# Kernel tuning notes

Hardware: AMD Instinct MI355X
Metric: run time of the kernel (lower is better)

Reference implementation:

```python
import jax, jax.numpy as jnp
import numpy as np

N_NODES = 100000


def _gcn_conv(x, W, b, src, dst, num_nodes):
    """PyG-style GCNConv: add self-loops, symmetric normalization, linear.
    x: [N, Fin], W: [Fin, Fout], b: [Fout], src/dst: [E] (already include self-loops).
    """
    h = x @ W  # [N, Fout] transform first (PyG order), keeps edge traffic at Fout width
    ones = jnp.ones(dst.shape[0], dtype=h.dtype)
    deg = jax.ops.segment_sum(ones, dst, num_segments=num_nodes)  # degree of A+I
    dinv = jnp.where(deg > 0, jax.lax.rsqrt(deg), 0.0)
    norm = dinv[src] * dinv[dst]  # [E]
    msg = h[src] * norm[:, None]  # [E, Fout] gather + scale
    out = jax.ops.segment_sum(msg, dst, num_segments=num_nodes)  # scatter-add
    return out + b


def setup_inputs() -> dict:
    key = jax.random.key(0)
    k1, k2, k3, k4, k5 = jax.random.split(key, 5)
    input_dim, hidden_dim, embedding_dim = 128, 64, 32
    x = jax.random.normal(k1, (N_NODES, input_dim), dtype=jnp.float32)
    edge_index = jax.random.randint(k2, (2, 1600000), 0, N_NODES, dtype=jnp.int32)
    # Glorot-like init for weights
    W1 = jax.random.normal(k3, (input_dim, hidden_dim), dtype=jnp.float32) / np.sqrt(input_dim)
    b1 = jnp.zeros((hidden_dim,), dtype=jnp.float32)
    W2 = jax.random.normal(k4, (hidden_dim, embedding_dim), dtype=jnp.float32) / np.sqrt(hidden_dim)
    b2 = jnp.zeros((embedding_dim,), dtype=jnp.float32)
    return {"x": x, "edge_index": edge_index, "W1": W1, "b1": b1, "W2": W2, "b2": b2}


def reference(x, edge_index, W1, b1, W2, b2):
    num_nodes = x.shape[0]
    loop = jnp.arange(num_nodes, dtype=edge_index.dtype)
    src = jnp.concatenate([edge_index[0], loop])  # add self-loops (PyG default)
    dst = jnp.concatenate([edge_index[1], loop])
    h = _gcn_conv(x, W1, b1, src, dst, num_nodes)
    h = jax.nn.relu(h)
    z = _gcn_conv(h, W2, b2, src, dst, num_nodes)
    return z
```

## Files before the change

### kernel.cpp

```cpp
#include <hip/hip_runtime.h>
#include <hip/hip_bf16.h>


#define MAXBUCK 512
#define CURSTRIDE 16

typedef unsigned int uint32;

__device__ __forceinline__ void fma4(float4& a, float s, const float4& w) {
    a.x = fmaf(s, w.x, a.x); a.y = fmaf(s, w.y, a.y);
    a.z = fmaf(s, w.z, a.z); a.w = fmaf(s, w.w, a.w);
}
__device__ __forceinline__ uint32 bf16rn(float f) {
    uint32 u = __float_as_uint(f);
    return (u + 0x7fffu + ((u >> 16) & 1u)) >> 16;
}
__device__ __forceinline__ float bflo(uint32 v) { return __uint_as_float(v << 16); }
__device__ __forceinline__ float bfhi(uint32 v) { return __uint_as_float(v & 0xffff0000u); }

__global__ void k_initcur(int* __restrict__ cursor, int nbuck, int cap) {
    int i = blockIdx.x * blockDim.x + threadIdx.x;
    if (i < nbuck) cursor[i * CURSTRIDE] = i * cap;
}

__global__ __launch_bounds__(1024) void k_bin(const int* __restrict__ src,
                                              const int* __restrict__ dst, int E,
                                              int nbuck, int cap,
                                              int* __restrict__ cursor,
                                              uint32* __restrict__ pairs) {
    __shared__ int hist[MAXBUCK];
    __shared__ int base_l[MAXBUCK];
    __shared__ int cur[MAXBUCK];
    int t = threadIdx.x;
    int e0 = blockIdx.x * 4096;
    for (int i = t; i < MAXBUCK; i += 1024) { hist[i] = 0; cur[i] = 0; }
    __syncthreads();
    for (int i = t; i < 4096; i += 1024) {
        int e = e0 + i;
        if (e < E) atomicAdd(&hist[dst[e] >> 8], 1);
    }
    __syncthreads();
    for (int i = t; i < nbuck; i += 1024)
        base_l[i] = hist[i] ? atomicAdd(&cursor[i * CURSTRIDE], hist[i]) : 0;
    __syncthreads();
    for (int i = t; i < 4096; i += 1024) {
        int e = e0 + i;
        if (e < E) {
            int d = dst[e];
            int b = d >> 8;
            int p = atomicAdd(&cur[b], 1);
            int idx = base_l[b] + p;
            if (idx < (b + 1) * cap)
                pairs[idx] = (uint32)src[e] | ((uint32)(d & 255) << 24);
        }
    }
}

__global__ __launch_bounds__(1024) void k_fill2(const uint32* __restrict__ pairs,
                                                const int* __restrict__ bucket_end,
                                                int cap, int N,
                                                int* __restrict__ srclist,
                                                int* __restrict__ rowstart,
                                                int* __restrict__ cnt,
                                                float* __restrict__ dinv) {
    __shared__ int hist[256];
    __shared__ int sh[256];
    __shared__ int rs_ex[256];
    __shared__ int cur[256];
    int b = blockIdx.x;
    int t = threadIdx.x;
    int start = b * cap;
    int end = min(bucket_end[b * CURSTRIDE], start + cap);
    int node0 = b << 8;

    if (t < 256) { hist[t] = 0; cur[t] = 0; }
    __syncthreads();
    for (int e = start + t; e < end; e += 1024)
        atomicAdd(&hist[pairs[e] >> 24], 1);
    __syncthreads();
    int v = 0;
    if (t < 256) { v = hist[t]; sh[t] = v; }
    __syncthreads();
    for (int off = 1; off < 256; off <<= 1) {
        int tmp = 0;
        if (t < 256 && t >= off) tmp = sh[t - off];
        __syncthreads();
        if (t < 256) sh[t] += tmp;
        __syncthreads();
    }
    if (t < 256) {
        rs_ex[t] = sh[t] - v;
        int node = node0 + t;
        if (node < N) {
            rowstart[node] = start + rs_ex[t];
            cnt[node] = v;
            dinv[node] = rsqrtf((float)(v + 1));
        }
    }
    __syncthreads();
    for (int e = start + t; e < end; e += 1024) {
        uint32 pr = pairs[e];
        int dl = pr >> 24;
        int p = atomicAdd(&cur[dl], 1);
        srclist[start + rs_ex[dl] + p] = (int)(pr & 0x00FFFFFFu);
    }
}

__global__ __launch_bounds__(256) void k_gemm1(const float* __restrict__ x,
                                               const float* __restrict__ W1,
                                               const float* __restrict__ dinv,
                                               uint32* __restrict__ h1b, int n) {
    __shared__ float W1s[128 * 64];
    __shared__ float xs[32][132];
    int t = threadIdx.x;
    const float4* W1v = (const float4*)W1;
    float4* W1sv = (float4*)W1s;
    for (int i = t; i < 2048; i += 256) W1sv[i] = W1v[i];
    int node0 = blockIdx.x * 32;
    const float4* xv = (const float4*)x;
    for (int i = t; i < 1024; i += 256) {
        int nl = i >> 5, kq = i & 31;
        int node = node0 + nl;
        float4 v = make_float4(0.f, 0.f, 0.f, 0.f);
        if (node < n) v = xv[(size_t)node * 32 + kq];
        *(float4*)&xs[nl][kq * 4] = v;
    }
    __syncthreads();

    int tx = t & 15;
    int ty = t >> 4;
    int na = ty * 2, nb = na + 1;
    float4 acc0 = make_float4(0.f, 0.f, 0.f, 0.f);
    float4 acc1 = make_float4(0.f, 0.f, 0.f, 0.f);
    const float4* W1sq = (const float4*)W1s;
#pragma unroll 4
    for (int kq = 0; kq < 32; kq++) {
        float4 xa = *(const float4*)&xs[na][kq * 4];
        float4 xb = *(const float4*)&xs[nb][kq * 4];
        float4 w0 = W1sq[(kq * 4 + 0) * 16 + tx];
        float4 w1 = W1sq[(kq * 4 + 1) * 16 + tx];
        float4 w2 = W1sq[(kq * 4 + 2) * 16 + tx];
        float4 w3 = W1sq[(kq * 4 + 3) * 16 + tx];
        fma4(acc0, xa.x, w0); fma4(acc0, xa.y, w1);
        fma4(acc0, xa.z, w2); fma4(acc0, xa.w, w3);
        fma4(acc1, xb.x, w0); fma4(acc1, xb.y, w1);
        fma4(acc1, xb.z, w2); fma4(acc1, xb.w, w3);
    }
    int nA = node0 + na, nB = node0 + nb;
    if (nA < n) {
        float di = dinv[nA];
        uint2 pk = make_uint2(bf16rn(acc0.x * di) | (bf16rn(acc0.y * di) << 16),
                              bf16rn(acc0.z * di) | (bf16rn(acc0.w * di) << 16));
        ((uint2*)h1b)[(size_t)nA * 16 + tx] = pk;
    }
    if (nB < n) {
        float di = dinv[nB];
        uint2 pk = make_uint2(bf16rn(acc1.x * di) | (bf16rn(acc1.y * di) << 16),
                              bf16rn(acc1.z * di) | (bf16rn(acc1.w * di) << 16));
        ((uint2*)h1b)[(size_t)nB * 16 + tx] = pk;
    }
}

__global__ __launch_bounds__(256) void k_gather_l1(const int* __restrict__ rowstart,
                                                   const int* __restrict__ cnt,
                                                   const int* __restrict__ srclist,
                                                   const uint32* __restrict__ h1b,
                                                   const float* __restrict__ dinv,
                                                   const float* __restrict__ b1,
                                                   const float* __restrict__ W2,
                                                   unsigned short* __restrict__ h2b, int n) {
    __shared__ __align__(16) float W2s[64 * 32];
    __shared__ __align__(16) float hb[8][64];
    int t = threadIdx.x;
    {
        const float4* W2v = (const float4*)W2;
        float4* W2sv = (float4*)W2s;
        W2sv[t] = W2v[t];
        W2sv[t + 256] = W2v[t + 256];
    }
    int wid = t >> 6, lane = t & 63;
    int nodeA = blockIdx.x * 8 + wid * 2;
    int nodeB = nodeA + 1;
    bool validA = (nodeA < n), validB = (nodeB < n);
    int j = lane & 15, q = lane >> 4;

    int rowA = 0, mA = 0, rowB = 0, mB = 0;
    float diA = 0.0f, diB = 0.0f;
    uint2 svA = make_uint2(0u, 0u), svB = make_uint2(0u, 0u);
    const uint2* h1v = (const uint2*)h1b;
    if (validA) { rowA = rowstart[nodeA]; mA = cnt[nodeA]; diA = dinv[nodeA];
                  svA = h1v[(size_t)nodeA * 16 + j]; }
    if (validB) { rowB = rowstart[nodeB]; mB = cnt[nodeB]; diB = dinv[nodeB];
                  svB = h1v[(size_t)nodeB * 16 + j]; }
    int mA0 = min(64, mA), mB0 = min(64, mB);
    int sidxA = (lane < mA0) ? srclist[rowA + lane] : 0;
    int sidxB = (lane < mB0) ? srclist[rowB + lane] : 0;

    float aA0 = 0.f, aA1 = 0.f, aA2 = 0.f, aA3 = 0.f;
    float aB0 = 0.f, aB1 = 0.f, aB2 = 0.f, aB3 = 0.f;
    int jjA = 0, jjB = 0;
    for (; jjA + 16 <= mA0 && jjB + 16 <= mB0; jjA += 16, jjB += 16) {
        int sA0 = __shfl(sidxA, jjA + q),      sA1 = __shfl(sidxA, jjA + 4 + q);
        int sA2 = __shfl(sidxA, jjA + 8 + q),  sA3 = __shfl(sidxA, jjA + 12 + q);
        int sB0 = __shfl(sidxB, jjB + q),      sB1 = __shfl(sidxB, jjB + 4 + q);
        int sB2 = __shfl(sidxB, jjB + 8 + q),  sB3 = __shfl(sidxB, jjB + 12 + q);
        uint2 vA0 = h1v[(size_t)sA0 * 16 + j], vA1 = h1v[(size_t)sA1 * 16 + j];
        uint2 vA2 = h1v[(size_t)sA2 * 16 + j], vA3 = h1v[(size_t)sA3 * 16 + j];
        uint2 vB0 = h1v[(size_t)sB0 * 16 + j], vB1 = h1v[(size_t)sB1 * 16 + j];
        uint2 vB2 = h1v[(size_t)sB2 * 16 + j], vB3 = h1v[(size_t)sB3 * 16 + j];
        aA0 += (bflo(vA0.x) + bflo(vA1.x)) + (bflo(vA2.x) + bflo(vA3.x));
        aA1 += (bfhi(vA0.x) + bfhi(vA1.x)) + (bfhi(vA2.x) + bfhi(vA3.x));
        aA2 += (bflo(vA0.y) + bflo(vA1.y)) + (bflo(vA2.y) + bflo(vA3.y));
        aA3 += (bfhi(vA0.y) + bfhi(vA1.y)) + (bfhi(vA2.y) + bfhi(vA3.y));
        aB0 += (bflo(vB0.x) + bflo(vB1.x)) + (bflo(vB2.x) + bflo(vB3.x));
        aB1 += (bfhi(vB0.x) + bfhi(vB1.x)) + (bfhi(vB2.x) + bfhi(vB3.x));
        aB2 += (bflo(vB0.y) + bflo(vB1.y)) + (bflo(vB2.y) + bflo(vB3.y));
        aB3 += (bfhi(vB0.y) + bfhi(vB1.y)) + (bfhi(vB2.y) + bfhi(vB3.y));
    }
    for (; jjA + 8 <= mA0 && jjB + 8 <= mB0; jjA += 8, jjB += 8) {
        int sA0 = __shfl(sidxA, jjA + q), sA1 = __shfl(sidxA, jjA + 4 + q);
        int sB0 = __shfl(sidxB, jjB + q), sB1 = __shfl(sidxB, jjB + 4 + q);
        uint2 vA0 = h1v[(size_t)sA0 * 16 + j], vA1 = h1v[(size_t)sA1 * 16 + j];
        uint2 vB0 = h1v[(size_t)sB0 * 16 + j], vB1 = h1v[(size_t)sB1 * 16 + j];
        aA0 += bflo(vA0.x) + bflo(vA1.x);
        aA1 += bfhi(vA0.x) + bfhi(vA1.x);
        aA2 += bflo(vA0.y) + bflo(vA1.y);
        aA3 += bfhi(vA0.y) + bfhi(vA1.y);
        aB0 += bflo(vB0.x) + bflo(vB1.x);
        aB1 += bfhi(vB0.x) + bfhi(vB1.x);
        aB2 += bflo(vB0.y) + bflo(vB1.y);
        aB3 += bfhi(vB0.y) + bfhi(vB1.y);
    }
    for (; jjA + 8 <= mA0; jjA += 8) {
        int s0 = __shfl(sidxA, jjA + q), s1 = __shfl(sidxA, jjA + 4 + q);
        uint2 v0 = h1v[(size_t)s0 * 16 + j], v1 = h1v[(size_t)s1 * 16 + j];
        aA0 += bflo(v0.x) + bflo(v1.x);
        aA1 += bfhi(v0.x) + bfhi(v1.x);
        aA2 += bflo(v0.y) + bflo(v1.y);
        aA3 += bfhi(v0.y) + bfhi(v1.y);
    }
    for (; jjA < mA0; jjA += 4) {
        int jidx = jjA + q;
        int s = __shfl(sidxA, min(jidx, mA0 - 1));
        uint2 v = h1v[(size_t)s * 16 + j];
        if (jidx < mA0) {
            aA0 += bflo(v.x); aA1 += bfhi(v.x);
            aA2 += bflo(v.y); aA3 += bfhi(v.y);
        }
    }
    for (; jjB + 8 <= mB0; jjB += 8) {
        int s0 = __shfl(sidxB, jjB + q), s1 = __shfl(sidxB, jjB + 4 + q);
        uint2 v0 = h1v[(size_t)s0 * 16 + j], v1 = h1v[(size_t)s1 * 16 + j];
        aB0 += bflo(v0.x) + bflo(v1.x);
        aB1 += bfhi(v0.x) + bfhi(v1.x);
        aB2 += bflo(v0.y) + bflo(v1.y);
        aB3 += bfhi(v0.y) + bfhi(v1.y);
    }
    for (; jjB < mB0; jjB += 4) {
        int jidx = jjB + q;
        int s = __shfl(sidxB, min(jidx, mB0 - 1));
        uint2 v = h1v[(size_t)s * 16 + j];
        if (jidx < mB0) {
            aB0 += bflo(v.x); aB1 += bfhi(v.x);
            aB2 += bflo(v.y); aB3 += bfhi(v.y);
        }
    }
    for (int j0 = 64; j0 < mA; j0 += 64) {
        int m = min(64, mA - j0);
        int sb = (lane < m) ? srclist[rowA + j0 + lane] : 0;
        int jj = 0;
        for (; jj + 8 <= m; jj += 8) {
            int s0 = __shfl(sb, jj + q), s1 = __shfl(sb, jj + 4 + q);
            uint2 v0 = h1v[(size_t)s0 * 16 + j], v1 = h1v[(size_t)s1 * 16 + j];
            aA0 += bflo(v0.x) + bflo(v1.x);
            aA1 += bfhi(v0.x) + bfhi(v1.x);
            aA2 += bflo(v0.y) + bflo(v1.y);
            aA3 += bfhi(v0.y) + bfhi(v1.y);
        }
        for (; jj < m; jj += 4) {
            int jidx = jj + q;
            int s = __shfl(sb, min(jidx, m - 1));
            uint2 v = h1v[(size_t)s * 16 + j];
            if (jidx < m) {
                aA0 += bflo(v.x); aA1 += bfhi(v.x);
                aA2 += bflo(v.y); aA3 += bfhi(v.y);
            }
        }
    }
    for (int j0 = 64; j0 < mB; j0 += 64) {
        int m = min(64, mB - j0);
        int sb = (lane < m) ? srclist[rowB + j0 + lane] : 0;
        int jj = 0;
        for (; jj + 8 <= m; jj += 8) {
            int s0 = __shfl(sb, jj + q), s1 = __shfl(sb, jj + 4 + q);
            uint2 v0 = h1v[(size_t)s0 * 16 + j], v1 = h1v[(size_t)s1 * 16 + j];
            aB0 += bflo(v0.x) + bflo(v1.x);
            aB1 += bfhi(v0.x) + bfhi(v1.x);
            aB2 += bflo(v0.y) + bflo(v1.y);
            aB3 += bfhi(v0.y) + bfhi(v1.y);
        }
        for (; jj < m; jj += 4) {
            int jidx = jj + q;
            int s = __shfl(sb, min(jidx, m - 1));
            uint2 v = h1v[(size_t)s * 16 + j];
            if (jidx < m) {
                aB0 += bflo(v.x); aB1 += bfhi(v.x);
                aB2 += bflo(v.y); aB3 += bfhi(v.y);
            }
        }
    }

    aA0 += __shfl_xor(aA0, 16); aA0 += __shfl_xor(aA0, 32);
    aA1 += __shfl_xor(aA1, 16); aA1 += __shfl_xor(aA1, 32);
    aA2 += __shfl_xor(aA2, 16); aA2 += __shfl_xor(aA2, 32);
    aA3 += __shfl_xor(aA3, 16); aA3 += __shfl_xor(aA3, 32);
    aB0 += __shfl_xor(aB0, 16); aB0 += __shfl_xor(aB0, 32);
    aB1 += __shfl_xor(aB1, 16); aB1 += __shfl_xor(aB1, 32);
    aB2 += __shfl_xor(aB2, 16); aB2 += __shfl_xor(aB2, 32);
    aB3 += __shfl_xor(aB3, 16); aB3 += __shfl_xor(aB3, 32);
    if (validA && q == 0) {
        float4 bq = ((const float4*)b1)[j];
        float4 hv;
        hv.x = fmaxf((aA0 + bflo(svA.x)) * diA + bq.x, 0.0f);
        hv.y = fmaxf((aA1 + bfhi(svA.x)) * diA + bq.y, 0.0f);
        hv.z = fmaxf((aA2 + bflo(svA.y)) * diA + bq.z, 0.0f);
        hv.w = fmaxf((aA3 + bfhi(svA.y)) * diA + bq.w, 0.0f);
        *(float4*)&hb[wid * 2][4 * j] = hv;
    }
    if (validB && q == 0) {
        float4 bq = ((const float4*)b1)[j];
        float4 hv;
        hv.x = fmaxf((aB0 + bflo(svB.x)) * diB + bq.x, 0.0f);
        hv.y = fmaxf((aB1 + bfhi(svB.x)) * diB + bq.y, 0.0f);
        hv.z = fmaxf((aB2 + bflo(svB.y)) * diB + bq.z, 0.0f);
        hv.w = fmaxf((aB3 + bfhi(svB.y)) * diB + bq.w, 0.0f);
        *(float4*)&hb[wid * 2 + 1][4 * j] = hv;
    }
    __syncthreads();
    int c = lane & 31, half = lane >> 5;
    int k0 = half * 32;
    if (validA) {
        float s = 0.0f;
        const float4* hb4 = (const float4*)&hb[wid * 2][k0];
#pragma unroll
        for (int kk = 0; kk < 8; kk++) {
            float4 h4 = hb4[kk];
            int kb = k0 + kk * 4;
            s = fmaf(h4.x, W2s[(kb + 0) * 32 + c], s);
            s = fmaf(h4.y, W2s[(kb + 1) * 32 + c], s);
            s = fmaf(h4.z, W2s[(kb + 2) * 32 + c], s);
            s = fmaf(h4.w, W2s[(kb + 3) * 32 + c], s);
        }
        s += __shfl_xor(s, 32);
        if (half == 0) h2b[(size_t)nodeA * 32 + c] = (unsigned short)bf16rn(s * diA);
    }
    if (validB) {
        float s = 0.0f;
        const float4* hb4 = (const float4*)&hb[wid * 2 + 1][k0];
#pragma unroll
        for (int kk = 0; kk < 8; kk++) {
            float4 h4 = hb4[kk];
            int kb = k0 + kk * 4;
            s = fmaf(h4.x, W2s[(kb + 0) * 32 + c], s);
            s = fmaf(h4.y, W2s[(kb + 1) * 32 + c], s);
            s = fmaf(h4.z, W2s[(kb + 2) * 32 + c], s);
            s = fmaf(h4.w, W2s[(kb + 3) * 32 + c], s);
        }
        s += __shfl_xor(s, 32);
        if (half == 0) h2b[(size_t)nodeB * 32 + c] = (unsigned short)bf16rn(s * diB);
    }
}

__global__ __launch_bounds__(256) void k_gather_l2(const int* __restrict__ rowstart,
                                                   const int* __restrict__ cnt,
                                                   const int* __restrict__ srclist,
                                                   const uint32* __restrict__ h2b,
                                                   const float* __restrict__ dinv,
                                                   const float* __restrict__ b2v,
                                                   float* __restrict__ out, int n) {
    int t = threadIdx.x;
    int wid = t >> 6, lane = t & 63;
    int nodeA = blockIdx.x * 8 + wid * 2;
    if (nodeA >= n) return;
    int nodeB = nodeA + 1;
    bool validB = (nodeB < n);
    int j = lane & 7, o = lane >> 3;

    int rowA = rowstart[nodeA], mA = cnt[nodeA];
    float diA = dinv[nodeA];
    int rowB = 0, mB = 0;
    float diB = 0.0f;
    const uint2* h2v = (const uint2*)h2b;
    uint2 svA = h2v[(size_t)nodeA * 8 + j];
    uint2 svB = make_uint2(0u, 0u);
    if (validB) { rowB = rowstart[nodeB]; mB = cnt[nodeB]; diB = dinv[nodeB];
                  svB = h2v[(size_t)nodeB * 8 + j]; }
    int mA0 = min(64, mA), mB0 = min(64, mB);
    int sidxA = (lane < mA0) ? srclist[rowA + lane] : 0;
    int sidxB = (lane < mB0) ? srclist[rowB + lane] : 0;

    float aA0 = 0.f, aA1 = 0.f, aA2 = 0.f, aA3 = 0.f;
    float aB0 = 0.f, aB1 = 0.f, aB2 = 0.f, aB3 = 0.f;
    int jjA = 0, jjB = 0;
    for (; jjA + 16 <= mA0 && jjB + 16 <= mB0; jjA += 16, jjB += 16) {
        int sA0 = __shfl(sidxA, jjA + o), sA1 = __shfl(sidxA, jjA + 8 + o);
        int sB0 = __shfl(sidxB, jjB + o), sB1 = __shfl(sidxB, jjB + 8 + o);
        uint2 vA0 = h2v[(size_t)sA0 * 8 + j], vA1 = h2v[(size_t)sA1 * 8 + j];
        uint2 vB0 = h2v[(size_t)sB0 * 8 + j], vB1 = h2v[(size_t)sB1 * 8 + j];
        aA0 += bflo(vA0.x) + bflo(vA1.x);
        aA1 += bfhi(vA0.x) + bfhi(vA1.x);
        aA2 += bflo(vA0.y) + bflo(vA1.y);
        aA3 += bfhi(vA0.y) + bfhi(vA1.y);
        aB0 += bflo(vB0.x) + bflo(vB1.x);
        aB1 += bfhi(vB0.x) + bfhi(vB1.x);
        aB2 += bflo(vB0.y) + bflo(vB1.y);
        aB3 += bfhi(vB0.y) + bfhi(vB1.y);
    }
    for (; jjA + 8 <= mA0 && jjB + 8 <= mB0; jjA += 8, jjB += 8) {
        int sA0 = __shfl(sidxA, jjA + o);
        int sB0 = __shfl(sidxB, jjB + o);
        uint2 vA0 = h2v[(size_t)sA0 * 8 + j];
        uint2 vB0 = h2v[(size_t)sB0 * 8 + j];
        aA0 += bflo(vA0.x); aA1 += bfhi(vA0.x);
        aA2 += bflo(vA0.y); aA3 += bfhi(vA0.y);
        aB0 += bflo(vB0.x); aB1 += bfhi(vB0.x);
        aB2 += bflo(vB0.y); aB3 += bfhi(vB0.y);
    }
    for (; jjA + 8 <= mA0; jjA += 8) {
        int s0 = __shfl(sidxA, jjA + o);
        uint2 v0 = h2v[(size_t)s0 * 8 + j];
        aA0 += bflo(v0.x); aA1 += bfhi(v0.x);
        aA2 += bflo(v0.y); aA3 += bfhi(v0.y);
    }
    if (jjA < mA0) {
        int jidx = jjA + o;
        int s = __shfl(sidxA, min(jidx, mA0 - 1));
        uint2 v = h2v[(size_t)s * 8 + j];
        if (jidx < mA0) {
            aA0 += bflo(v.x); aA1 += bfhi(v.x);
            aA2 += bflo(v.y); aA3 += bfhi(v.y);
        }
    }
    for (; jjB + 8 <= mB0; jjB += 8) {
        int s0 = __shfl(sidxB, jjB + o);
        uint2 v0 = h2v[(size_t)s0 * 8 + j];
        aB0 += bflo(v0.x); aB1 += bfhi(v0.x);
        aB2 += bflo(v0.y); aB3 += bfhi(v0.y);
    }
    if (jjB < mB0) {
        int jidx = jjB + o;
        int s = __shfl(sidxB, min(jidx, mB0 - 1));
        uint2 v = h2v[(size_t)s * 8 + j];
        if (jidx < mB0) {
            aB0 += bflo(v.x); aB1 += bfhi(v.x);
            aB2 += bflo(v.y); aB3 += bfhi(v.y);
        }
    }
    for (int j0 = 64; j0 < mA; j0 += 64) {
        int m = min(64, mA - j0);
        int sb = (lane < m) ? srclist[rowA + j0 + lane] : 0;
        int jj = 0;
        for (; jj + 8 <= m; jj += 8) {
            int s0 = __shfl(sb, jj + o);
            uint2 v0 = h2v[(size_t)s0 * 8 + j];
            aA0 += bflo(v0.x); aA1 += bfhi(v0.x);
            aA2 += bflo(v0.y); aA3 += bfhi(v0.y);
        }
        if (jj < m) {
            int jidx = jj + o;
            int s = __shfl(sb, min(jidx, m - 1));
            uint2 v = h2v[(size_t)s * 8 + j];
            if (jidx < m) {
                aA0 += bflo(v.x); aA1 += bfhi(v.x);
                aA2 += bflo(v.y); aA3 += bfhi(v.y);
            }
        }
    }
    for (int j0 = 64; j0 < mB; j0 += 64) {
        int m = min(64, mB - j0);
        int sb = (lane < m) ? srclist[rowB + j0 + lane] : 0;
        int jj = 0;
        for (; jj + 8 <= m; jj += 8) {
            int s0 = __shfl(sb, jj + o);
            uint2 v0 = h2v[(size_t)s0 * 8 + j];
            aB0 += bflo(v0.x); aB1 += bfhi(v0.x);
            aB2 += bflo(v0.y); aB3 += bfhi(v0.y);
        }
        if (jj < m) {
            int jidx = jj + o;
            int s = __shfl(sb, min(jidx, m - 1));
            uint2 v = h2v[(size_t)s * 8 + j];
            if (jidx < m) {
                aB0 += bflo(v.x); aB1 += bfhi(v.x);
                aB2 += bflo(v.y); aB3 += bfhi(v.y);
            }
        }
    }

    a_reduce:
    aA0 += __shfl_xor(aA0, 8); aA0 += __shfl_xor(aA0, 16); aA0 += __shfl_xor(aA0, 32);
    aA1 += __shfl_xor(aA1, 8); aA1 += __shfl_xor(aA1, 16); aA1 += __shfl_xor(aA1, 32);
    aA2 += __shfl_xor(aA2, 8); aA2 += __shfl_xor(aA2, 16); aA2 += __shfl_xor(aA2, 32);
    aA3 += __shfl_xor(aA3, 8); aA3 += __shfl_xor(aA3, 16); aA3 += __shfl_xor(aA3, 32);
    aB0 += __shfl_xor(aB0, 8); aB0 += __shfl_xor(aB0, 16); aB0 += __shfl_xor(aB0, 32);
    aB1 += __shfl_xor(aB1, 8); aB1 += __shfl_xor(aB1, 16); aB1 += __shfl_xor(aB1, 32);
    aB2 += __shfl_xor(aB2, 8); aB2 += __shfl_xor(aB2, 16); aB2 += __shfl_xor(aB2, 32);
    aB3 += __shfl_xor(aB3, 8); aB3 += __shfl_xor(aB3, 16); aB3 += __shfl_xor(aB3, 32);
    if (o == 0) {
        float4 bq = ((const float4*)b2v)[j];
        float4 ov;
        ov.x = (aA0 + bflo(svA.x)) * diA + bq.x;
        ov.y = (aA1 + bfhi(svA.x)) * diA + bq.y;
        ov.z = (aA2 + bflo(svA.y)) * diA + bq.z;
        ov.w = (aA3 + bfhi(svA.y)) * diA + bq.w;
        ((float4*)out)[(size_t)nodeA * 8 + j] = ov;
        if (validB) {
            float4 ob;
            ob.x = (aB0 + bflo(svB.x)) * diB + bq.x;
            ob.y = (aB1 + bfhi(svB.x)) * diB + bq.y;
            ob.z = (aB2 + bflo(svB.y)) * diB + bq.z;
            ob.w = (aB3 + bfhi(svB.y)) * diB + bq.w;
            ((float4*)out)[(size_t)nodeB * 8 + j] = ob;
        }
    }
}

extern "C" void kernel_launch(void* const* d_in, const int* in_sizes, int n_in,
                              void* d_out, int out_size, void* d_ws, size_t ws_size,
                              hipStream_t stream) {
    const float* x  = (const float*)d_in[0];
    const int*   ei = (const int*)d_in[1];
    const float* W1 = (const float*)d_in[2];
    const float* b1 = (const float*)d_in[3];
    const float* W2 = (const float*)d_in[4];
    const float* b2 = (const float*)d_in[5];
    float* out = (float*)d_out;

    const int N = in_sizes[0] / 128;
    const int E = in_sizes[1] / 2;
    const int* src = ei;
    const int* dst = ei + E;
    const int nbuck = (N + 255) >> 8;

    int mean = (E + nbuck - 1) / nbuck;
    int cap = (mean + (mean >> 3) + 256 + 63) & ~63;
    size_t region = (size_t)nbuck * cap;

    char* p = (char*)d_ws;
    uint32* pairs      = (uint32*)p;    p += region * 4;
    int* srclist       = (int*)p;       p += region * 4;
    uint32* h1b        = (uint32*)p;    p += (size_t)N * 64 * 2;
    uint32* h2b        = (uint32*)p;    p += (size_t)N * 32 * 2;
    int* cursor        = (int*)p;       p += MAXBUCK * CURSTRIDE * 4;
    int* rowstart      = (int*)p;       p += (size_t)N * 4;
    int* cnt           = (int*)p;       p += (size_t)N * 4;
    float* dinv        = (float*)p;     p += (size_t)N * 4;

    k_initcur<<<(nbuck + 255) / 256, 256, 0, stream>>>(cursor, nbuck, cap);
    k_bin<<<(E + 4095) / 4096, 1024, 0, stream>>>(src, dst, E, nbuck, cap, cursor, pairs);
    k_fill2<<<nbuck, 1024, 0, stream>>>(pairs, cursor, cap, N, srclist, rowstart, cnt, dinv);

    k_gemm1<<<(N + 31) / 32, 256, 0, stream>>>(x, W1, dinv, h1b, N);
    k_gather_l1<<<(N + 7) / 8, 256, 0, stream>>>(rowstart, cnt, srclist, h1b, dinv,
                                                 b1, W2, (unsigned short*)h2b, N);
    k_gather_l2<<<(N + 7) / 8, 256, 0, stream>>>(rowstart, cnt, srclist, h2b, dinv,
                                                 b2, out, N);
}
```

Baseline: 235.7 us.

## Halve gemm1 shared memory, cache dst in LDS, replace cursor init kernel with memset

k_gemm1 now stages W1 and x in two K-halves, cutting shared memory per block from about 49KB to about 25KB so more blocks can be resident, at the cost of an extra sync phase. k_bin keeps the dst values in shared memory so it does not re-read them from global memory. The cursor-init kernel is replaced by a memset, with bucket offsets added inside k_bin, and k_fill2 now reads per-bucket counts instead of end positions.

Measured after the change: 234.3 us. No clear change (-0.6%).

```diff
diff --git a/kernel.cpp b/kernel.cpp
--- a/kernel.cpp
+++ b/kernel.cpp
@@ -17,11 +17,6 @@
 }
 __device__ __forceinline__ float bflo(uint32 v) { return __uint_as_float(v << 16); }
 __device__ __forceinline__ float bfhi(uint32 v) { return __uint_as_float(v & 0xffff0000u); }
-
-__global__ void k_initcur(int* __restrict__ cursor, int nbuck, int cap) {
-    int i = blockIdx.x * blockDim.x + threadIdx.x;
-    if (i < nbuck) cursor[i * CURSTRIDE] = i * cap;
-}
 
 __global__ __launch_bounds__(1024) void k_bin(const int* __restrict__ src,
                                               const int* __restrict__ dst, int E,
@@ -31,22 +26,27 @@
     __shared__ int hist[MAXBUCK];
     __shared__ int base_l[MAXBUCK];
     __shared__ int cur[MAXBUCK];
+    __shared__ int dloc[4096];
     int t = threadIdx.x;
     int e0 = blockIdx.x * 4096;
     for (int i = t; i < MAXBUCK; i += 1024) { hist[i] = 0; cur[i] = 0; }
-    __syncthreads();
-    for (int i = t; i < 4096; i += 1024) {
-        int e = e0 + i;
-        if (e < E) atomicAdd(&hist[dst[e] >> 8], 1);
-    }
-    __syncthreads();
-    for (int i = t; i < nbuck; i += 1024)
-        base_l[i] = hist[i] ? atomicAdd(&cursor[i * CURSTRIDE], hist[i]) : 0;
     __syncthreads();
     for (int i = t; i < 4096; i += 1024) {
         int e = e0 + i;
         if (e < E) {
             int d = dst[e];
+            dloc[i] = d;
+            atomicAdd(&hist[d >> 8], 1);
+        }
+    }
+    __syncthreads();
+    for (int i = t; i < nbuck; i += 1024)
+        base_l[i] = hist[i] ? (i * cap + atomicAdd(&cursor[i * CURSTRIDE], hist[i])) : 0;
+    __syncthreads();
+    for (int i = t; i < 4096; i += 1024) {
+        int e = e0 + i;
+        if (e < E) {
+            int d = dloc[i];
             int b = d >> 8;
             int p = atomicAdd(&cur[b], 1);
             int idx = base_l[b] + p;
@@ -57,7 +57,7 @@
 }
 
 __global__ __launch_bounds__(1024) void k_fill2(const uint32* __restrict__ pairs,
-                                                const int* __restrict__ bucket_end,
+                                                const int* __restrict__ bucket_cnt,
                                                 int cap, int N,
                                                 int* __restrict__ srclist,
                                                 int* __restrict__ rowstart,
@@ -70,7 +70,7 @@
     int b = blockIdx.x;
     int t = threadIdx.x;
     int start = b * cap;
-    int end = min(bucket_end[b * CURSTRIDE], start + cap);
+    int end = start + min(bucket_cnt[b * CURSTRIDE], cap);
     int node0 = b << 8;
 
     if (t < 256) { hist[t] = 0; cur[t] = 0; }
@@ -110,41 +110,45 @@
                                                const float* __restrict__ W1,
                                                const float* __restrict__ dinv,
                                                uint32* __restrict__ h1b, int n) {
-    __shared__ float W1s[128 * 64];
-    __shared__ float xs[32][132];
+    __shared__ float W1s[64 * 64];
+    __shared__ float xs[32][68];
     int t = threadIdx.x;
-    const float4* W1v = (const float4*)W1;
-    float4* W1sv = (float4*)W1s;
-    for (int i = t; i < 2048; i += 256) W1sv[i] = W1v[i];
     int node0 = blockIdx.x * 32;
-    const float4* xv = (const float4*)x;
-    for (int i = t; i < 1024; i += 256) {
-        int nl = i >> 5, kq = i & 31;
-        int node = node0 + nl;
-        float4 v = make_float4(0.f, 0.f, 0.f, 0.f);
-        if (node < n) v = xv[(size_t)node * 32 + kq];
-        *(float4*)&xs[nl][kq * 4] = v;
-    }
-    __syncthreads();
-
     int tx = t & 15;
     int ty = t >> 4;
     int na = ty * 2, nb = na + 1;
     float4 acc0 = make_float4(0.f, 0.f, 0.f, 0.f);
     float4 acc1 = make_float4(0.f, 0.f, 0.f, 0.f);
+    const float4* W1v = (const float4*)W1;
+    const float4* xv = (const float4*)x;
+    float4* W1sv = (float4*)W1s;
     const float4* W1sq = (const float4*)W1s;
+
+#pragma unroll 1
+    for (int ph = 0; ph < 2; ph++) {
+        __syncthreads();
+        for (int i = t; i < 1024; i += 256) W1sv[i] = W1v[ph * 1024 + i];
+        for (int i = t; i < 512; i += 256) {
+            int nl = i >> 4, kq4 = i & 15;
+            int node = node0 + nl;
+            float4 v = make_float4(0.f, 0.f, 0.f, 0.f);
+            if (node < n) v = xv[(size_t)node * 32 + ph * 16 + kq4];
+            *(float4*)&xs[nl][kq4 * 4] = v;
+        }
+        __syncthreads();
 #pragma unroll 4
-    for (int kq = 0; kq < 32; kq++) {
-        float4 xa = *(const float4*)&xs[na][kq * 4];
-        float4 xb = *(const float4*)&xs[nb][kq * 4];
-        float4 w0 = W1sq[(kq * 4 + 0) * 16 + tx];
-        float4 w1 = W1sq[(kq * 4 + 1) * 16 + tx];
-        float4 w2 = W1sq[(kq * 4 + 2) * 16 + tx];
-        float4 w3 = W1sq[(kq * 4 + 3) * 16 + tx];
-        fma4(acc0, xa.x, w0); fma4(acc0, xa.y, w1);
-        fma4(acc0, xa.z, w2); fma4(acc0, xa.w, w3);
-        fma4(acc1, xb.x, w0); fma4(acc1, xb.y, w1);
-        fma4(acc1, xb.z, w2); fma4(acc1, xb.w, w3);
+        for (int kq = 0; kq < 16; kq++) {
+            float4 xa = *(const float4*)&xs[na][kq * 4];
+            float4 xb = *(const float4*)&xs[nb][kq * 4];
+            float4 w0 = W1sq[(kq * 4 + 0) * 16 + tx];
+            float4 w1 = W1sq[(kq * 4 + 1) * 16 + tx];
+            float4 w2 = W1sq[(kq * 4 + 2) * 16 + tx];
+            float4 w3 = W1sq[(kq * 4 + 3) * 16 + tx];
+            fma4(acc0, xa.x, w0); fma4(acc0, xa.y, w1);
+            fma4(acc0, xa.z, w2); fma4(acc0, xa.w, w3);
+            fma4(acc1, xb.x, w0); fma4(acc1, xb.y, w1);
+            fma4(acc1, xb.z, w2); fma4(acc1, xb.w, w3);
+        }
     }
     int nA = node0 + na, nB = node0 + nb;
     if (nA < n) {
@@ -497,7 +501,6 @@
         }
     }
 
-    a_reduce:
     aA0 += __shfl_xor(aA0, 8); aA0 += __shfl_xor(aA0, 16); aA0 += __shfl_xor(aA0, 32);
     aA1 += __shfl_xor(aA1, 8); aA1 += __shfl_xor(aA1, 16); aA1 += __shfl_xor(aA1, 32);
     aA2 += __shfl_xor(aA2, 8); aA2 += __shfl_xor(aA2, 16); aA2 += __shfl_xor(aA2, 32);
@@ -556,7 +559,7 @@
     int* cnt           = (int*)p;       p += (size_t)N * 4;
     float* dinv        = (float*)p;     p += (size_t)N * 4;
 
-    k_initcur<<<(nbuck + 255) / 256, 256, 0, stream>>>(cursor, nbuck, cap);
+    hipMemsetAsync(cursor, 0, (size_t)nbuck * CURSTRIDE * 4, stream);
     k_bin<<<(E + 4095) / 4096, 1024, 0, stream>>>(src, dst, E, nbuck, cap, cursor, pairs);
     k_fill2<<<nbuck, 1024, 0, stream>>>(pairs, cursor, cap, N, srclist, rowstart, cnt, dinv);
 
```
